# Kernel tuning notes

Measured on AMD Instinct MI355X. Metric: run time of the kernel, lower is better.

The kernel has to match this reference:

```python
import jax, jax.numpy as jnp
import numpy as np

IMAGE_SIZE = 512
STRIDES = (8, 16, 32)
W_SEG, W_DET, W_CLS = 1.0, 1.0, 0.5


def _bce_logits(x, y):
    # numerically stable binary cross entropy with logits (broadcasts y)
    return jnp.maximum(x, 0.0) - x * y + jnp.log1p(jnp.exp(-jnp.abs(x)))


def _focal_loss_mean(logits, targets, num_classes, alpha=0.25, gamma=2.0):
    # sigmoid focal loss; targets are class indices, -1 (or any negative) => all-background row
    t = jax.nn.one_hot(targets, num_classes, dtype=logits.dtype)
    p = jax.nn.sigmoid(logits)
    ce = _bce_logits(logits, t)
    p_t = p * t + (1.0 - p) * (1.0 - t)
    a_t = alpha * t + (1.0 - alpha) * (1.0 - t)
    return jnp.mean(a_t * (1.0 - p_t) ** gamma * ce)


def _det_scale_loss(cls_logits, reg_preds, cent_preds, boxes, labels, stride):
    B, Cp1, H, W = cls_logits.shape
    C = Cp1 - 1
    L = H * W
    cls = jnp.transpose(cls_logits, (0, 2, 3, 1))[..., 1:].reshape(B, L, C)
    reg = jnp.transpose(reg_preds, (0, 2, 3, 1)).reshape(B, L, 4)
    cent = cent_preds.reshape(B, L)
    xs = (jnp.arange(W, dtype=jnp.float32) + 0.5) * stride
    ys = (jnp.arange(H, dtype=jnp.float32) + 0.5) * stride
    gy, gx = jnp.meshgrid(ys, xs, indexing='ij')
    loc_x = gx.reshape(-1)
    loc_y = gy.reshape(-1)

    def per_image(cls_i, reg_i, cent_i, gb, gl):
        b = gb * IMAGE_SIZE  # [cx,cy,w,h] in pixels
        x0 = b[:, 0] - b[:, 2] * 0.5
        y0 = b[:, 1] - b[:, 3] * 0.5
        x1 = b[:, 0] + b[:, 2] * 0.5
        y1 = b[:, 1] + b[:, 3] * 0.5
        l = loc_x[:, None] - x0[None, :]
        t = loc_y[:, None] - y0[None, :]
        r = x1[None, :] - loc_x[:, None]
        btm = y1[None, :] - loc_y[:, None]
        ltrb = jnp.stack([l, t, r, btm], axis=-1)  # (L, N, 4)
        inside = jnp.min(ltrb, axis=-1) > 0
        area = (x1 - x0) * (y1 - y0)
        masked_area = jnp.where(inside, area[None, :], jnp.inf)
        idx = jnp.argmin(masked_area, axis=-1)  # min-area matched box per location
        pos = jnp.any(inside, axis=-1)
        cls_t = jnp.where(pos, gl[idx], -1)
        reg_t = jnp.take_along_axis(ltrb, idx[:, None, None], axis=1)[:, 0, :] / stride
        lr = reg_t[:, jnp.array([0, 2])]
        tb = reg_t[:, jnp.array([1, 3])]
        eps = 1e-6
        cen_t = jnp.sqrt(jnp.clip((jnp.min(lr, -1) / (jnp.max(lr, -1) + eps)) * (jnp.min(tb, -1) / (jnp.max(tb, -1) + eps)), 0.0, 1.0))
        cls_l = _focal_loss_mean(cls_i, cls_t, C)
        npos = jnp.sum(pos)
        d = reg_i - reg_t
        sl1 = jnp.mean(jnp.where(jnp.abs(d) < 1.0, 0.5 * d * d, jnp.abs(d) - 0.5), axis=-1)
        posf = pos.astype(jnp.float32)
        denom = jnp.maximum(npos, 1).astype(jnp.float32)
        reg_l = jnp.where(npos > 0, jnp.sum(sl1 * posf) / denom, 0.0)
        bce = _bce_logits(cent_i, cen_t)
        cen_l = jnp.where(npos > 0, jnp.sum(bce * posf) / denom, 0.0)
        return cls_l, reg_l, cen_l

    cl, rl, cel = jax.vmap(per_image)(cls, reg, cent, boxes, labels)
    return jnp.mean(cl), jnp.mean(rl), jnp.mean(cel)


def _total_loss(seg_logits, seg_mask, cls_list, reg_list, cen_list, boxes, labels, cls_pred, cls_target):
    # segmentation: BCE-with-logits, integer mask broadcast as float target over channels
    seg_t = seg_mask.astype(jnp.float32)[:, None, :, :]  # (B,1,H,W) broadcasts vs (B,C,H,W)
    seg_loss = jnp.mean(_bce_logits(seg_logits, seg_t))
    tot_cls = 0.0
    tot_reg = 0.0
    tot_cen = 0.0
    for s in range(3):
        cl, rl, cel = _det_scale_loss(cls_list[s], reg_list[s], cen_list[s], boxes, labels, STRIDES[s])
        tot_cls = tot_cls + cl
        tot_reg = tot_reg + rl
        tot_cen = tot_cen + cel
    n = 3.0
    det_loss = tot_cls / n + tot_reg / n + tot_cen / n
    cls_loss = _focal_loss_mean(cls_pred, cls_target, cls_pred.shape[-1])
    return W_SEG * seg_loss + W_DET * det_loss + W_CLS * cls_loss


def setup_inputs() -> dict:
    key = jax.random.key(0)
    ks = jax.random.split(key, 16)
    B = 32
    inp = {
        'seg_logits': jax.random.normal(ks[0], (B, 4, 512, 512), jnp.float32),
        'seg_mask': jax.random.randint(ks[1], (B, 512, 512), 0, 4, jnp.int32),
        'cls_logits_s0': jax.random.normal(ks[2], (B, 5, 64, 64), jnp.float32),
        'cls_logits_s1': jax.random.normal(ks[3], (B, 5, 32, 32), jnp.float32),
        'cls_logits_s2': jax.random.normal(ks[4], (B, 5, 16, 16), jnp.float32),
        'reg_preds_s0': jax.random.normal(ks[5], (B, 4, 64, 64), jnp.float32),
        'reg_preds_s1': jax.random.normal(ks[6], (B, 4, 32, 32), jnp.float32),
        'reg_preds_s2': jax.random.normal(ks[7], (B, 4, 16, 16), jnp.float32),
        'centerness_s0': jax.random.normal(ks[8], (B, 1, 64, 64), jnp.float32),
        'centerness_s1': jax.random.normal(ks[9], (B, 1, 32, 32), jnp.float32),
        'centerness_s2': jax.random.normal(ks[10], (B, 1, 16, 16), jnp.float32),
        'boxes': jax.random.uniform(ks[11], (B, 20, 4), jnp.float32),
        'labels': jax.random.randint(ks[12], (B, 20), 0, 4, jnp.int32),
        'cls_pred': jax.random.normal(ks[13], (B, 10), jnp.float32),
        'cls_target': jax.random.randint(ks[14], (B,), 0, 10, jnp.int32),
    }
    return inp


def reference(seg_logits, seg_mask, cls_logits_s0, cls_logits_s1, cls_logits_s2, reg_preds_s0, reg_preds_s1, reg_preds_s2, centerness_s0, centerness_s1, centerness_s2, boxes, labels, cls_pred, cls_target):
    return _total_loss(seg_logits, seg_mask,
                       (cls_logits_s0, cls_logits_s1, cls_logits_s2),
                       (reg_preds_s0, reg_preds_s1, reg_preds_s2),
                       (centerness_s0, centerness_s1, centerness_s2),
                       boxes, labels, cls_pred, cls_target)
```

## Files before the change

kernel.cpp:

```cpp
#include <hip/hip_runtime.h>
#include <math.h>

#define NB 32
#define SEG_BLOCKS 2048
#define DET_BLOCKS 96


__device__ __forceinline__ float bce_logits(float x, float y) {
    float a = fabsf(x);
    return fmaxf(x, 0.f) - x * y + __logf(1.f + __expf(-a));
}

__device__ __forceinline__ float focal_elt(float x, float t) {
    float p = 1.f / (1.f + __expf(-x));
    float ce = bce_logits(x, t);
    float p_t = (t > 0.5f) ? p : (1.f - p);
    float a_t = (t > 0.5f) ? 0.25f : 0.75f;
    float om = 1.f - p_t;
    return a_t * om * om * ce;
}

template <int N>
__device__ void blk_reduce_arr(float* v) {
    __shared__ float sm[N][4];
    int lane = threadIdx.x & 63;
    int wid  = threadIdx.x >> 6;
#pragma unroll
    for (int j = 0; j < N; j++) {
        float x = v[j];
#pragma unroll
        for (int off = 32; off > 0; off >>= 1) x += __shfl_down(x, off, 64);
        if (lane == 0) sm[j][wid] = x;
    }
    __syncthreads();
    if (threadIdx.x == 0) {
#pragma unroll
        for (int j = 0; j < N; j++) {
            float s = 0.f;
#pragma unroll
            for (int w = 0; w < 4; w++) s += sm[j][w];
            v[j] = s;
        }
    }
}


__global__ __launch_bounds__(256) void fused_kernel(
        const float* __restrict__ seg_logits, const int* __restrict__ mask,
        const float* __restrict__ cls0, const float* __restrict__ cls1, const float* __restrict__ cls2,
        const float* __restrict__ reg0, const float* __restrict__ reg1, const float* __restrict__ reg2,
        const float* __restrict__ cen0, const float* __restrict__ cen1, const float* __restrict__ cen2,
        const float* __restrict__ boxes, const int* __restrict__ labels,
        float* __restrict__ segpart, float* __restrict__ detc) {

    if (blockIdx.x < DET_BLOCKS) {
        const int s = blockIdx.x >> 5;
        const int b = blockIdx.x & 31;
        int Wd, shift, L; float stride;
        const float *cls, *reg, *cen;
        if (s == 0)      { Wd = 64; shift = 6; L = 4096; stride = 8.f;  cls = cls0; reg = reg0; cen = cen0; }
        else if (s == 1) { Wd = 32; shift = 5; L = 1024; stride = 16.f; cls = cls1; reg = reg1; cen = cen1; }
        else             { Wd = 16; shift = 4; L = 256;  stride = 32.f; cls = cls2; reg = reg2; cen = cen2; }

        __shared__ float sx0[20], sy0[20], sx1[20], sy1[20], sar[20];
        __shared__ int   slb[20];
        if (threadIdx.x < 20) {
            int k = threadIdx.x;
            const float* bb = boxes + (b * 20 + k) * 4;
            float cx = bb[0] * 512.f, cy = bb[1] * 512.f;
            float w  = bb[2] * 512.f, h  = bb[3] * 512.f;
            float x0 = cx - 0.5f * w, y0 = cy - 0.5f * h;
            float x1 = cx + 0.5f * w, y1 = cy + 0.5f * h;
            sx0[k] = x0; sy0[k] = y0; sx1[k] = x1; sy1[k] = y1;
            sar[k] = (x1 - x0) * (y1 - y0);
            slb[k] = labels[b * 20 + k];
        }
        __syncthreads();

        const float* clsb = cls + (size_t)b * 5 * L;
        const float* regb = reg + (size_t)b * 4 * L;
        const float* cenb = cen + (size_t)b * L;
        const float inv = 1.f / stride;

        float cls_s = 0.f, reg_s = 0.f, cen_s = 0.f, np = 0.f;
        for (int l = threadIdx.x; l < L; l += 256) {
            float lx = ((l & (Wd - 1)) + 0.5f) * stride;
            float ly = ((l >> shift)   + 0.5f) * stride;
            int bk = -1; float ba = INFINITY;
            float bl = 0.f, btp = 0.f, brr = 0.f, bbt = 0.f;
#pragma unroll
            for (int k = 0; k < 20; k++) {
                float li = lx - sx0[k], ti = ly - sy0[k];
                float ri = sx1[k] - lx, bi = sy1[k] - ly;
                float mn = fminf(fminf(li, ti), fminf(ri, bi));
                if (mn > 0.f && sar[k] < ba) {
                    ba = sar[k]; bk = k;
                    bl = li; btp = ti; brr = ri; bbt = bi;
                }
            }
            int tl = (bk >= 0) ? slb[bk] : -1;
#pragma unroll
            for (int c = 0; c < 4; c++) {
                float x = clsb[(c + 1) * L + l];
                cls_s += focal_elt(x, (c == tl) ? 1.f : 0.f);
            }
            if (bk >= 0) {
                float r0 = bl * inv, r1 = btp * inv, r2 = brr * inv, r3 = bbt * inv;
                float d0 = regb[0 * L + l] - r0;
                float d1 = regb[1 * L + l] - r1;
                float d2 = regb[2 * L + l] - r2;
                float d3 = regb[3 * L + l] - r3;
                float a0 = fabsf(d0), a1 = fabsf(d1), a2 = fabsf(d2), a3 = fabsf(d3);
                float sl = (a0 < 1.f ? 0.5f * d0 * d0 : a0 - 0.5f)
                         + (a1 < 1.f ? 0.5f * d1 * d1 : a1 - 0.5f)
                         + (a2 < 1.f ? 0.5f * d2 * d2 : a2 - 0.5f)
                         + (a3 < 1.f ? 0.5f * d3 * d3 : a3 - 0.5f);
                reg_s += 0.25f * sl;
                float mnlr = fminf(r0, r2), mxlr = fmaxf(r0, r2);
                float mntb = fminf(r1, r3), mxtb = fmaxf(r1, r3);
                float v = (mnlr / (mxlr + 1e-6f)) * (mntb / (mxtb + 1e-6f));
                v = fminf(fmaxf(v, 0.f), 1.f);
                float ct = sqrtf(v);
                cen_s += bce_logits(cenb[l], ct);
                np += 1.f;
            }
        }

        float v4[4] = {cls_s, reg_s, cen_s, np};
        blk_reduce_arr<4>(v4);
        if (threadIdx.x == 0) {
            float cls_l = v4[0] / (L * 4.f);
            float npos  = v4[3];
            float denom = fmaxf(npos, 1.f);
            float reg_l = (npos > 0.f) ? v4[1] / denom : 0.f;
            float cen_l = (npos > 0.f) ? v4[2] / denom : 0.f;
            detc[blockIdx.x] = (cls_l + reg_l + cen_l) * (1.f / (float)DET_BLOCKS);
        }
        __syncthreads();
    }

    const int HW  = 512 * 512;
    const int QPI = HW / 4;
    const int TOTQ = NB * QPI;
    int tid = blockIdx.x * 256 + threadIdx.x;
    float acc = 0.f;
    for (int q = tid; q < TOTQ; q += SEG_BLOCKS * 256) {
        int b   = q >> 16;
        int hwq = q & 65535;
        const int4 m4 = ((const int4*)(mask + (size_t)b * HW))[hwq];
        float ty0 = (float)m4.x, ty1 = (float)m4.y, ty2 = (float)m4.z, ty3 = (float)m4.w;
        const float4* base = (const float4*)(seg_logits + (size_t)b * 4 * HW);
#pragma unroll
        for (int c = 0; c < 4; c++) {
            float4 x4 = base[c * QPI + hwq];
            acc += bce_logits(x4.x, ty0) + bce_logits(x4.y, ty1)
                 + bce_logits(x4.z, ty2) + bce_logits(x4.w, ty3);
        }
    }
    float v[1] = {acc};
    blk_reduce_arr<1>(v);
    if (threadIdx.x == 0) segpart[blockIdx.x] = v[0];
}


__global__ __launch_bounds__(256) void final_kernel(
        const float* __restrict__ segpart, const float* __restrict__ detc,
        const float* __restrict__ cls_pred, const int* __restrict__ cls_target,
        float* __restrict__ out) {
    const float seg_scale = 1.f / 33554432.f;
    const float cls_scale = 0.5f / 320.f;
    float acc = 0.f;
    for (int i = threadIdx.x; i < SEG_BLOCKS; i += 256) acc += segpart[i] * seg_scale;
    if (threadIdx.x < DET_BLOCKS) acc += detc[threadIdx.x];
    for (int e = threadIdx.x; e < NB * 10; e += 256) {
        int i = e / 10, c = e - i * 10;
        acc += cls_scale * focal_elt(cls_pred[e], (cls_target[i] == c) ? 1.f : 0.f);
    }
    float v[1] = {acc};
    blk_reduce_arr<1>(v);
    if (threadIdx.x == 0) out[0] = v[0];
}


extern "C" void kernel_launch(void* const* d_in, const int* in_sizes, int n_in,
                              void* d_out, int out_size, void* d_ws, size_t ws_size,
                              hipStream_t stream) {
    const float* seg_logits = (const float*)d_in[0];
    const int*   seg_mask   = (const int*)d_in[1];
    const float* cls0 = (const float*)d_in[2];
    const float* cls1 = (const float*)d_in[3];
    const float* cls2 = (const float*)d_in[4];
    const float* reg0 = (const float*)d_in[5];
    const float* reg1 = (const float*)d_in[6];
    const float* reg2 = (const float*)d_in[7];
    const float* cen0 = (const float*)d_in[8];
    const float* cen1 = (const float*)d_in[9];
    const float* cen2 = (const float*)d_in[10];
    const float* boxes  = (const float*)d_in[11];
    const int*   labels = (const int*)d_in[12];
    const float* cls_pred   = (const float*)d_in[13];
    const int*   cls_target = (const int*)d_in[14];

    float* ws      = (float*)d_ws;
    float* segpart = ws;
    float* detc    = ws + SEG_BLOCKS;

    fused_kernel<<<SEG_BLOCKS, 256, 0, stream>>>(seg_logits, seg_mask,
                                                 cls0, cls1, cls2,
                                                 reg0, reg1, reg2,
                                                 cen0, cen1, cen2,
                                                 boxes, labels, segpart, detc);
    final_kernel<<<1, 256, 0, stream>>>(segpart, detc, cls_pred, cls_target,
                                        (float*)d_out);
}
```

Before: 248.0 us.

## Split fused loss kernel into dedicated seg and det kernels with staged mask

```diff
diff --git a/kernel.cpp b/kernel.cpp
--- a/kernel.cpp
+++ b/kernel.cpp
@@ -2,8 +2,10 @@
 #include <math.h>
 
 #define NB 32
+#define DET_BLOCKS 96
 #define SEG_BLOCKS 2048
-#define DET_BLOCKS 96
+
+typedef float fvec4 __attribute__((ext_vector_type(4)));
 
 
 __device__ __forceinline__ float bce_logits(float x, float y) {
@@ -45,121 +47,145 @@
 }
 
 
-__global__ __launch_bounds__(256) void fused_kernel(
-        const float* __restrict__ seg_logits, const int* __restrict__ mask,
+__global__ __launch_bounds__(256, 8) void seg_kernel(
+        const float* __restrict__ logits, const int* __restrict__ mask,
+        float* __restrict__ partial) {
+    const int HW  = 512 * 512;
+    const int QPI = HW / 4;
+    __shared__ fvec4 smask[1024];
+
+    const int t = threadIdx.x;
+    const size_t qb = (size_t)blockIdx.x * 1024;
+    const int b    = (int)(qb >> 16);
+    const int hwq0 = (int)(qb & 65535);
+
+    const int4* mq = (const int4*)(mask + (size_t)b * HW) + hwq0;
+#pragma unroll
+    for (int i = 0; i < 4; i++) {
+        const int4 m = mq[i * 256 + t];
+        fvec4 f; f.x = (float)m.x; f.y = (float)m.y;
+        f.z = (float)m.z; f.w = (float)m.w;
+        smask[i * 256 + t] = f;
+    }
+    __syncthreads();
+
+    float acc = 0.f;
+    const fvec4* xq = (const fvec4*)(logits + (size_t)b * 4 * HW) + hwq0;
+#pragma unroll 1
+    for (int c = 0; c < 4; c++) {
+        const fvec4* xc = xq + (size_t)c * QPI;
+        fvec4 x0 = __builtin_nontemporal_load(xc + 0 * 256 + t);
+        fvec4 x1 = __builtin_nontemporal_load(xc + 1 * 256 + t);
+        fvec4 x2 = __builtin_nontemporal_load(xc + 2 * 256 + t);
+        fvec4 x3 = __builtin_nontemporal_load(xc + 3 * 256 + t);
+        fvec4 t0 = smask[0 * 256 + t];
+        fvec4 t1 = smask[1 * 256 + t];
+        fvec4 t2 = smask[2 * 256 + t];
+        fvec4 t3 = smask[3 * 256 + t];
+        acc += bce_logits(x0.x, t0.x) + bce_logits(x0.y, t0.y)
+             + bce_logits(x0.z, t0.z) + bce_logits(x0.w, t0.w);
+        acc += bce_logits(x1.x, t1.x) + bce_logits(x1.y, t1.y)
+             + bce_logits(x1.z, t1.z) + bce_logits(x1.w, t1.w);
+        acc += bce_logits(x2.x, t2.x) + bce_logits(x2.y, t2.y)
+             + bce_logits(x2.z, t2.z) + bce_logits(x2.w, t2.w);
+        acc += bce_logits(x3.x, t3.x) + bce_logits(x3.y, t3.y)
+             + bce_logits(x3.z, t3.z) + bce_logits(x3.w, t3.w);
+    }
+
+    float v[1] = {acc};
+    blk_reduce_arr<1>(v);
+    if (t == 0) partial[blockIdx.x] = v[0];
+}
+
+
+__global__ __launch_bounds__(256) void det_kernel(
         const float* __restrict__ cls0, const float* __restrict__ cls1, const float* __restrict__ cls2,
         const float* __restrict__ reg0, const float* __restrict__ reg1, const float* __restrict__ reg2,
         const float* __restrict__ cen0, const float* __restrict__ cen1, const float* __restrict__ cen2,
         const float* __restrict__ boxes, const int* __restrict__ labels,
-        float* __restrict__ segpart, float* __restrict__ detc) {
-
-    if (blockIdx.x < DET_BLOCKS) {
-        const int s = blockIdx.x >> 5;
-        const int b = blockIdx.x & 31;
-        int Wd, shift, L; float stride;
-        const float *cls, *reg, *cen;
-        if (s == 0)      { Wd = 64; shift = 6; L = 4096; stride = 8.f;  cls = cls0; reg = reg0; cen = cen0; }
-        else if (s == 1) { Wd = 32; shift = 5; L = 1024; stride = 16.f; cls = cls1; reg = reg1; cen = cen1; }
-        else             { Wd = 16; shift = 4; L = 256;  stride = 32.f; cls = cls2; reg = reg2; cen = cen2; }
-
-        __shared__ float sx0[20], sy0[20], sx1[20], sy1[20], sar[20];
-        __shared__ int   slb[20];
-        if (threadIdx.x < 20) {
-            int k = threadIdx.x;
-            const float* bb = boxes + (b * 20 + k) * 4;
-            float cx = bb[0] * 512.f, cy = bb[1] * 512.f;
-            float w  = bb[2] * 512.f, h  = bb[3] * 512.f;
-            float x0 = cx - 0.5f * w, y0 = cy - 0.5f * h;
-            float x1 = cx + 0.5f * w, y1 = cy + 0.5f * h;
-            sx0[k] = x0; sy0[k] = y0; sx1[k] = x1; sy1[k] = y1;
-            sar[k] = (x1 - x0) * (y1 - y0);
-            slb[k] = labels[b * 20 + k];
-        }
-        __syncthreads();
-
-        const float* clsb = cls + (size_t)b * 5 * L;
-        const float* regb = reg + (size_t)b * 4 * L;
-        const float* cenb = cen + (size_t)b * L;
-        const float inv = 1.f / stride;
-
-        float cls_s = 0.f, reg_s = 0.f, cen_s = 0.f, np = 0.f;
-        for (int l = threadIdx.x; l < L; l += 256) {
-            float lx = ((l & (Wd - 1)) + 0.5f) * stride;
-            float ly = ((l >> shift)   + 0.5f) * stride;
-            int bk = -1; float ba = INFINITY;
-            float bl = 0.f, btp = 0.f, brr = 0.f, bbt = 0.f;
-#pragma unroll
-            for (int k = 0; k < 20; k++) {
-                float li = lx - sx0[k], ti = ly - sy0[k];
-                float ri = sx1[k] - lx, bi = sy1[k] - ly;
-                float mn = fminf(fminf(li, ti), fminf(ri, bi));
-                if (mn > 0.f && sar[k] < ba) {
-                    ba = sar[k]; bk = k;
-                    bl = li; btp = ti; brr = ri; bbt = bi;
-                }
+        float* __restrict__ detc) {
+    const int s = blockIdx.x >> 5;
+    const int b = blockIdx.x & 31;
+    int Wd, shift, L; float stride;
+    const float *cls, *reg, *cen;
+    if (s == 0)      { Wd = 64; shift = 6; L = 4096; stride = 8.f;  cls = cls0; reg = reg0; cen = cen0; }
+    else if (s == 1) { Wd = 32; shift = 5; L = 1024; stride = 16.f; cls = cls1; reg = reg1; cen = cen1; }
+    else             { Wd = 16; shift = 4; L = 256;  stride = 32.f; cls = cls2; reg = reg2; cen = cen2; }
+
+    __shared__ float sx0[20], sy0[20], sx1[20], sy1[20], sar[20];
+    __shared__ int   slb[20];
+    if (threadIdx.x < 20) {
+        int k = threadIdx.x;
+        const float* bb = boxes + (b * 20 + k) * 4;
+        float cx = bb[0] * 512.f, cy = bb[1] * 512.f;
+        float w  = bb[2] * 512.f, h  = bb[3] * 512.f;
+        float x0 = cx - 0.5f * w, y0 = cy - 0.5f * h;
+        float x1 = cx + 0.5f * w, y1 = cy + 0.5f * h;
+        sx0[k] = x0; sy0[k] = y0; sx1[k] = x1; sy1[k] = y1;
+        sar[k] = (x1 - x0) * (y1 - y0);
+        slb[k] = labels[b * 20 + k];
+    }
+    __syncthreads();
+
+    const float* clsb = cls + (size_t)b * 5 * L;
+    const float* regb = reg + (size_t)b * 4 * L;
+    const float* cenb = cen + (size_t)b * L;
+    const float inv = 1.f / stride;
+
+    float cls_s = 0.f, reg_s = 0.f, cen_s = 0.f, np = 0.f;
+    for (int l = threadIdx.x; l < L; l += 256) {
+        float lx = ((l & (Wd - 1)) + 0.5f) * stride;
+        float ly = ((l >> shift)   + 0.5f) * stride;
+        int bk = -1; float ba = INFINITY;
+        float bl = 0.f, btp = 0.f, brr = 0.f, bbt = 0.f;
+#pragma unroll
+        for (int k = 0; k < 20; k++) {
+            float li = lx - sx0[k], ti = ly - sy0[k];
+            float ri = sx1[k] - lx, bi = sy1[k] - ly;
+            float mn = fminf(fminf(li, ti), fminf(ri, bi));
+            if (mn > 0.f && sar[k] < ba) {
+                ba = sar[k]; bk = k;
+                bl = li; btp = ti; brr = ri; bbt = bi;
             }
-            int tl = (bk >= 0) ? slb[bk] : -1;
-#pragma unroll
-            for (int c = 0; c < 4; c++) {
-                float x = clsb[(c + 1) * L + l];
-                cls_s += focal_elt(x, (c == tl) ? 1.f : 0.f);
-            }
-            if (bk >= 0) {
-                float r0 = bl * inv, r1 = btp * inv, r2 = brr * inv, r3 = bbt * inv;
-                float d0 = regb[0 * L + l] - r0;
-                float d1 = regb[1 * L + l] - r1;
-                float d2 = regb[2 * L + l] - r2;
-                float d3 = regb[3 * L + l] - r3;
-                float a0 = fabsf(d0), a1 = fabsf(d1), a2 = fabsf(d2), a3 = fabsf(d3);
-                float sl = (a0 < 1.f ? 0.5f * d0 * d0 : a0 - 0.5f)
-                         + (a1 < 1.f ? 0.5f * d1 * d1 : a1 - 0.5f)
-                         + (a2 < 1.f ? 0.5f * d2 * d2 : a2 - 0.5f)
-                         + (a3 < 1.f ? 0.5f * d3 * d3 : a3 - 0.5f);
-                reg_s += 0.25f * sl;
-                float mnlr = fminf(r0, r2), mxlr = fmaxf(r0, r2);
-                float mntb = fminf(r1, r3), mxtb = fmaxf(r1, r3);
-                float v = (mnlr / (mxlr + 1e-6f)) * (mntb / (mxtb + 1e-6f));
-                v = fminf(fmaxf(v, 0.f), 1.f);
-                float ct = sqrtf(v);
-                cen_s += bce_logits(cenb[l], ct);
-                np += 1.f;
-            }
-        }
-
-        float v4[4] = {cls_s, reg_s, cen_s, np};
-        blk_reduce_arr<4>(v4);
-        if (threadIdx.x == 0) {
-            float cls_l = v4[0] / (L * 4.f);
-            float npos  = v4[3];
-            float denom = fmaxf(npos, 1.f);
-            float reg_l = (npos > 0.f) ? v4[1] / denom : 0.f;
-            float cen_l = (npos > 0.f) ? v4[2] / denom : 0.f;
-            detc[blockIdx.x] = (cls_l + reg_l + cen_l) * (1.f / (float)DET_BLOCKS);
-        }
-        __syncthreads();
-    }
-
-    const int HW  = 512 * 512;
-    const int QPI = HW / 4;
-    const int TOTQ = NB * QPI;
-    int tid = blockIdx.x * 256 + threadIdx.x;
-    float acc = 0.f;
-    for (int q = tid; q < TOTQ; q += SEG_BLOCKS * 256) {
-        int b   = q >> 16;
-        int hwq = q & 65535;
-        const int4 m4 = ((const int4*)(mask + (size_t)b * HW))[hwq];
-        float ty0 = (float)m4.x, ty1 = (float)m4.y, ty2 = (float)m4.z, ty3 = (float)m4.w;
-        const float4* base = (const float4*)(seg_logits + (size_t)b * 4 * HW);
+        }
+        int tl = (bk >= 0) ? slb[bk] : -1;
 #pragma unroll
         for (int c = 0; c < 4; c++) {
-            float4 x4 = base[c * QPI + hwq];
-            acc += bce_logits(x4.x, ty0) + bce_logits(x4.y, ty1)
-                 + bce_logits(x4.z, ty2) + bce_logits(x4.w, ty3);
-        }
-    }
-    float v[1] = {acc};
-    blk_reduce_arr<1>(v);
-    if (threadIdx.x == 0) segpart[blockIdx.x] = v[0];
+            float x = clsb[(c + 1) * L + l];
+            cls_s += focal_elt(x, (c == tl) ? 1.f : 0.f);
+        }
+        if (bk >= 0) {
+            float r0 = bl * inv, r1 = btp * inv, r2 = brr * inv, r3 = bbt * inv;
+            float d0 = regb[0 * L + l] - r0;
+            float d1 = regb[1 * L + l] - r1;
+            float d2 = regb[2 * L + l] - r2;
+            float d3 = regb[3 * L + l] - r3;
+            float a0 = fabsf(d0), a1 = fabsf(d1), a2 = fabsf(d2), a3 = fabsf(d3);
+            float sl = (a0 < 1.f ? 0.5f * d0 * d0 : a0 - 0.5f)
+                     + (a1 < 1.f ? 0.5f * d1 * d1 : a1 - 0.5f)
+                     + (a2 < 1.f ? 0.5f * d2 * d2 : a2 - 0.5f)
+                     + (a3 < 1.f ? 0.5f * d3 * d3 : a3 - 0.5f);
+            reg_s += 0.25f * sl;
+            float mnlr = fminf(r0, r2), mxlr = fmaxf(r0, r2);
+            float mntb = fminf(r1, r3), mxtb = fmaxf(r1, r3);
+            float v = (mnlr / (mxlr + 1e-6f)) * (mntb / (mxtb + 1e-6f));
+            v = fminf(fmaxf(v, 0.f), 1.f);
+            float ct = sqrtf(v);
+            cen_s += bce_logits(cenb[l], ct);
+            np += 1.f;
+        }
+    }
+
+    float v4[4] = {cls_s, reg_s, cen_s, np};
+    blk_reduce_arr<4>(v4);
+    if (threadIdx.x == 0) {
+        float cls_l = v4[0] / (L * 4.f);
+        float npos  = v4[3];
+        float denom = fmaxf(npos, 1.f);
+        float reg_l = (npos > 0.f) ? v4[1] / denom : 0.f;
+        float cen_l = (npos > 0.f) ? v4[2] / denom : 0.f;
+        detc[blockIdx.x] = (cls_l + reg_l + cen_l) * (1.f / (float)DET_BLOCKS);
+    }
 }
 
 
@@ -205,11 +231,11 @@
     float* segpart = ws;
     float* detc    = ws + SEG_BLOCKS;
 
-    fused_kernel<<<SEG_BLOCKS, 256, 0, stream>>>(seg_logits, seg_mask,
-                                                 cls0, cls1, cls2,
-                                                 reg0, reg1, reg2,
-                                                 cen0, cen1, cen2,
-                                                 boxes, labels, segpart, detc);
+    seg_kernel<<<SEG_BLOCKS, 256, 0, stream>>>(seg_logits, seg_mask, segpart);
+    det_kernel<<<DET_BLOCKS, 256, 0, stream>>>(cls0, cls1, cls2,
+                                               reg0, reg1, reg2,
+                                               cen0, cen1, cen2,
+                                               boxes, labels, detc);
     final_kernel<<<1, 256, 0, stream>>>(segpart, detc, cls_pred, cls_target,
                                         (float*)d_out);
 }
```

New measurement: 265.3 us. 7.0% more time.
